# Kernel optimization log

Hardware: AMD Instinct MI355X
Metric: run time of the kernel (lower is better)

Reference implementation:

```python
import jax, jax.numpy as jnp
import numpy as np

N = 100000
E = 400000
NFEAT, NHID, NOUT, NHEAD = 128, 64, 128, 4
HIDDEN = NHID * NHEAD  # 256
SLOPE = 0.2


def gat_conv(x, src, dst, W, a_src, a_dst, b, concat):
    """PyG-style GATConv (eval mode, self-loops already appended to src/dst).
    x: [N, Fin]; W: [Fin, H*C]; a_src/a_dst: [H, C]; b: [H*C] or [C]."""
    H, C = a_src.shape
    h = (x @ W).reshape(N, H, C)                      # [N,H,C]
    al_s = (h * a_src).sum(-1)                        # [N,H] per-node src score
    al_d = (h * a_dst).sum(-1)                        # [N,H] per-node dst score
    e = jax.nn.leaky_relu(al_s[src] + al_d[dst], SLOPE)  # [Et,H]
    # segment softmax over incoming edges of each dst node
    m = jax.ops.segment_max(e, dst, num_segments=N)
    m = jnp.where(jnp.isfinite(m), m, 0.0)
    ex = jnp.exp(e - m[dst])
    denom = jax.ops.segment_sum(ex, dst, num_segments=N)
    alpha = ex / (denom[dst] + 1e-16)                 # [Et,H]
    msg = alpha[:, :, None] * h[src]                  # [Et,H,C]
    out = jax.ops.segment_sum(msg, dst, num_segments=N)  # [N,H,C]
    out = out.reshape(N, H * C) if concat else out.mean(axis=1)
    return out + b


def setup_inputs() -> dict:
    key = jax.random.key(0)
    ks = jax.random.split(key, 16)
    x = jax.random.normal(ks[0], (N, NFEAT), dtype=jnp.float32)
    edge_index = jax.random.randint(ks[1], (2, E), 0, N, dtype=jnp.int64)
    s = 0.1
    inp = {
        'x': x, 'edge_index': edge_index,
        # layer 0: nfeat -> nhid x nhead (concat)
        'W0': jax.random.normal(ks[2], (NFEAT, HIDDEN), jnp.float32) * s,
        'as0': jax.random.normal(ks[3], (NHEAD, NHID), jnp.float32) * s,
        'ad0': jax.random.normal(ks[4], (NHEAD, NHID), jnp.float32) * s,
        'b0': jnp.zeros((HIDDEN,), jnp.float32),
        # layer 1: hidden -> nhid x nhead (concat)
        'W1': jax.random.normal(ks[5], (HIDDEN, HIDDEN), jnp.float32) * s,
        'as1': jax.random.normal(ks[6], (NHEAD, NHID), jnp.float32) * s,
        'ad1': jax.random.normal(ks[7], (NHEAD, NHID), jnp.float32) * s,
        'b1': jnp.zeros((HIDDEN,), jnp.float32),
        # output layer: hidden -> nout, heads=1, concat=False
        'W2': jax.random.normal(ks[8], (HIDDEN, NOUT), jnp.float32) * s,
        'as2': jax.random.normal(ks[9], (1, NOUT), jnp.float32) * s,
        'ad2': jax.random.normal(ks[10], (1, NOUT), jnp.float32) * s,
        'b2': jnp.zeros((NOUT,), jnp.float32),
    }
    return inp


def reference(x, edge_index, W0, as0, ad0, b0, W1, as1, ad1, b1, W2, as2, ad2, b2):
    # PyG GATConv adds self-loops by default; edge set is shared across layers.
    loop = jnp.arange(N, dtype=edge_index.dtype)
    src = jnp.concatenate([edge_index[0], loop])
    dst = jnp.concatenate([edge_index[1], loop])
    # dropout inactive in eval mode
    h = jax.nn.elu(gat_conv(x, src, dst, W0, as0, ad0, b0, concat=True))
    h = jax.nn.elu(gat_conv(h, src, dst, W1, as1, ad1, b1, concat=True))
    out = gat_conv(h, src, dst, W2, as2, ad2, b2, concat=False)
    return out
```

## Files before the change

### kernel.cpp

```cpp
#include <hip/hip_runtime.h>
#include <cmath>

#define NN 100000
#define EE 400000
#define ET (EE + NN)
#define SLOPE 0.2f

typedef __attribute__((ext_vector_type(8))) short short8;
typedef __attribute__((ext_vector_type(4))) float floatx4;

__device__ __forceinline__ float b2f(ushort u) {
    union { unsigned int i; float f; } v; v.i = ((unsigned int)u) << 16; return v.f;
}
__device__ __forceinline__ ushort f2b(float f) {
    union { float f; unsigned int i; } v; v.f = f;
    unsigned int r = v.i + 0x7FFFu + ((v.i >> 16) & 1u);
    return (ushort)(r >> 16);
}

__global__ __launch_bounds__(256) void count_deg(const int* __restrict__ ei, int* __restrict__ deg) {
    int e = blockIdx.x * 256 + threadIdx.x;
    if (e < EE) atomicAdd(&deg[ei[EE + e]], 1);
}

__global__ __launch_bounds__(256) void scan1(const int* __restrict__ deg, int* __restrict__ incl,
                                             int* __restrict__ bsums) {
    __shared__ int ts[256];
    int b = blockIdx.x, t = threadIdx.x;
    int base = b * 1024 + t * 4;
    int v[4];
#pragma unroll
    for (int i = 0; i < 4; i++) {
        int n = base + i;
        v[i] = (n < NN) ? (deg[n] + 1) : 0;
    }
    int s = 0;
#pragma unroll
    for (int i = 0; i < 4; i++) { s += v[i]; v[i] = s; }
    ts[t] = s;
    __syncthreads();
    for (int off = 1; off < 256; off <<= 1) {
        int x = (t >= off) ? ts[t - off] : 0;
        __syncthreads();
        ts[t] += x;
        __syncthreads();
    }
    int excl = ts[t] - s;
#pragma unroll
    for (int i = 0; i < 4; i++) {
        int n = base + i;
        if (n < NN) incl[n] = v[i] + excl;
    }
    if (t == 255) bsums[b] = ts[255];
}

__global__ __launch_bounds__(128) void scan2(int* __restrict__ bsums, int nblk) {
    __shared__ int ts[128];
    int t = threadIdx.x;
    int v = (t < nblk) ? bsums[t] : 0;
    ts[t] = v;
    __syncthreads();
    for (int off = 1; off < 128; off <<= 1) {
        int x = (t >= off) ? ts[t - off] : 0;
        __syncthreads();
        ts[t] += x;
        __syncthreads();
    }
    if (t < nblk) bsums[t] = ts[t] - v;
}

__global__ __launch_bounds__(256) void scan3(const int* __restrict__ incl, const int* __restrict__ deg,
                                             const int* __restrict__ bsums, int* __restrict__ row_ptr,
                                             int* __restrict__ cursor) {
    int n = blockIdx.x * 256 + threadIdx.x;
    if (n < NN) {
        int rp = incl[n] - (deg[n] + 1) + bsums[n >> 10];
        row_ptr[n] = rp;
        cursor[n] = rp;
    }
    if (n == 0) row_ptr[NN] = ET;
}

__global__ __launch_bounds__(256) void scatter(const int* __restrict__ ei, int* __restrict__ cursor,
                                               int* __restrict__ col) {
    int e = blockIdx.x * 256 + threadIdx.x;
    if (e < EE) {
        int d = ei[EE + e];
        int p = atomicAdd(&cursor[d], 1);
        col[p] = ei[e];
    }
}

__global__ __launch_bounds__(256) void selfloop(const int* __restrict__ cursor, int* __restrict__ col) {
    int n = blockIdx.x * 256 + threadIdx.x;
    if (n < NN) col[cursor[n]] = n;
}

__global__ __launch_bounds__(256) void cast_to_bf16(const float* __restrict__ in,
                                                    ushort* __restrict__ out, int n4) {
    int i = blockIdx.x * 256 + threadIdx.x;
    if (i < n4) {
        float4 v = ((const float4*)in)[i];
        ushort4 o;
        o.x = f2b(v.x); o.y = f2b(v.y); o.z = f2b(v.z); o.w = f2b(v.w);
        ((ushort4*)out)[i] = o;
    }
}

__global__ __launch_bounds__(256) void transpose_cast(const float* __restrict__ W,
                                                      ushort* __restrict__ Wt, int K, int N) {
    int idx = blockIdx.x * 256 + threadIdx.x;
    if (idx < N * K) {
        int n = idx / K, k = idx % K;
        Wt[idx] = f2b(W[(size_t)k * N + n]);
    }
}

#define LP 40
__global__ __launch_bounds__(256) void gemm_bf16(const ushort* __restrict__ A,
                                                 const ushort* __restrict__ Bt,
                                                 ushort* __restrict__ C,
                                                 int M, int K, int N) {
    __shared__ ushort As[128 * LP];
    __shared__ ushort Bs[128 * LP];
    int tid = threadIdx.x;
    int bm = blockIdx.x * 128;
    int bn = blockIdx.y * 128;
    int wave = tid >> 6, lane = tid & 63;
    int wm = (wave >> 1) * 64, wn = (wave & 1) * 64;

    floatx4 acc[4][4];
#pragma unroll
    for (int i = 0; i < 4; i++)
#pragma unroll
        for (int j = 0; j < 4; j++) acc[i][j] = (floatx4)0.f;

    int r = tid >> 1;
    int c = (tid & 1) * 16;

    int frow = lane & 15;
    int kq = (lane >> 4) * 8;

    for (int k0 = 0; k0 < K; k0 += 32) {
        uint4 a0, a1;
        if (bm + r < M) {
            const uint4* ap = (const uint4*)(A + (size_t)(bm + r) * K + k0 + c);
            a0 = ap[0]; a1 = ap[1];
        } else {
            a0 = make_uint4(0, 0, 0, 0); a1 = a0;
        }
        *(uint4*)&As[r * LP + c]     = a0;
        *(uint4*)&As[r * LP + c + 8] = a1;

        const uint4* bp = (const uint4*)(Bt + (size_t)(bn + r) * K + k0 + c);
        *(uint4*)&Bs[r * LP + c]     = bp[0];
        *(uint4*)&Bs[r * LP + c + 8] = bp[1];

        __syncthreads();

        short8 afr[4], bfr[4];
#pragma unroll
        for (int i = 0; i < 4; i++)
            afr[i] = *(const short8*)&As[(wm + i * 16 + frow) * LP + kq];
#pragma unroll
        for (int j = 0; j < 4; j++)
            bfr[j] = *(const short8*)&Bs[(wn + j * 16 + frow) * LP + kq];
#pragma unroll
        for (int i = 0; i < 4; i++)
#pragma unroll
            for (int j = 0; j < 4; j++)
                acc[i][j] = __builtin_amdgcn_mfma_f32_16x16x32_bf16(afr[i], bfr[j], acc[i][j], 0, 0, 0);

        __syncthreads();
    }

    int ccol = bn + wn + (lane & 15);
    int crow = bm + wm + (lane >> 4) * 4;
#pragma unroll
    for (int i = 0; i < 4; i++) {
#pragma unroll
        for (int reg = 0; reg < 4; reg++) {
            int row = crow + i * 16 + reg;
            if (row < M) {
#pragma unroll
                for (int j = 0; j < 4; j++)
                    C[(size_t)row * N + ccol + j * 16] = f2b(acc[i][j][reg]);
            }
        }
    }
}

template <int H, int HC>
__global__ __launch_bounds__(256) void scores_k(const ushort* __restrict__ h,
                                                const float* __restrict__ a_s,
                                                const float* __restrict__ a_d,
                                                float* __restrict__ als,
                                                float* __restrict__ ald) {
    constexpr int CP = HC / 64;
    constexpr int GS = 64 / H;
    int wv = threadIdx.x >> 6, lane = threadIdx.x & 63;
    int n = blockIdx.x * 4 + wv;
    if (n >= NN) return;
    const uint* p = (const uint*)(h + (size_t)n * HC + lane * CP);
    float s = 0.f, d = 0.f;
#pragma unroll
    for (int q = 0; q < CP / 2; q++) {
        uint u = p[q];
        int ch = lane * CP + 2 * q;
        float v0 = b2f((ushort)(u & 0xffff)), v1 = b2f((ushort)(u >> 16));
        s += v0 * a_s[ch] + v1 * a_s[ch + 1];
        d += v0 * a_d[ch] + v1 * a_d[ch + 1];
    }
#pragma unroll
    for (int off = 1; off < GS; off <<= 1) {
        s += __shfl_xor(s, off, 64);
        d += __shfl_xor(d, off, 64);
    }
    if ((lane & (GS - 1)) == 0) {
        int head = lane / GS;
        als[n * H + head] = s;
        ald[n * H + head] = d;
    }
}

template <int H, int HC, bool ELU_ACT, bool OUT_BF16>
__global__ __launch_bounds__(256) void aggregate(const ushort* __restrict__ hlin,
                                                 const float* __restrict__ als,
                                                 const float* __restrict__ ald,
                                                 const int* __restrict__ row_ptr,
                                                 const int* __restrict__ col,
                                                 const float* __restrict__ bias,
                                                 void* __restrict__ outv) {
    constexpr int CP = HC / 64;
    constexpr int GS = 64 / H;
    int wv = threadIdx.x >> 6, lane = threadIdx.x & 63;
    int dst = blockIdx.x * 4 + wv;
    if (dst >= NN) return;
    int rs = row_ptr[dst], re = row_ptr[dst + 1];
    int deg = re - rs;
    int eg = lane & (GS - 1);
    int head = lane / GS;
    float ad = ald[dst * H + head];

    float acc[CP];
#pragma unroll
    for (int j = 0; j < CP; j++) acc[j] = 0.f;

    uint laneoff = (uint)(lane * CP);

    if (deg <= GS) {
        int src = 0;
        float s = -1e30f;
        if (eg < deg) {
            src = col[rs + eg];
            float sc = als[src * H + head] + ad;
            s = sc > 0.f ? sc : SLOPE * sc;
        }
        float m = s;
#pragma unroll
        for (int off = 1; off < GS; off <<= 1) m = fmaxf(m, __shfl_xor(m, off, 64));
        float e = (eg < deg) ? __expf(s - m) : 0.f;
        float sum = e;
#pragma unroll
        for (int off = 1; off < GS; off <<= 1) sum += __shfl_xor(sum, off, 64);
        float w = e * (1.0f / (sum + 1e-16f));

        int hbase = head * GS;
        int d = 0;
        for (; d + 4 <= deg; d += 4) {
            int s0 = __shfl(src, d, 64),     s1 = __shfl(src, d + 1, 64);
            int s2 = __shfl(src, d + 2, 64), s3 = __shfl(src, d + 3, 64);
            float w0 = __shfl(w, hbase + d, 64),     w1 = __shfl(w, hbase + d + 1, 64);
            float w2 = __shfl(w, hbase + d + 2, 64), w3 = __shfl(w, hbase + d + 3, 64);
            const uint* p0 = (const uint*)(hlin + (uint)s0 * HC + laneoff);
            const uint* p1 = (const uint*)(hlin + (uint)s1 * HC + laneoff);
            const uint* p2 = (const uint*)(hlin + (uint)s2 * HC + laneoff);
            const uint* p3 = (const uint*)(hlin + (uint)s3 * HC + laneoff);
            uint u0[CP / 2], u1[CP / 2], u2[CP / 2], u3[CP / 2];
#pragma unroll
            for (int q = 0; q < CP / 2; q++) { u0[q] = p0[q]; u1[q] = p1[q]; u2[q] = p2[q]; u3[q] = p3[q]; }
#pragma unroll
            for (int q = 0; q < CP / 2; q++) {
                acc[2*q]   += w0 * b2f((ushort)(u0[q] & 0xffff)) + w1 * b2f((ushort)(u1[q] & 0xffff))
                            + w2 * b2f((ushort)(u2[q] & 0xffff)) + w3 * b2f((ushort)(u3[q] & 0xffff));
                acc[2*q+1] += w0 * b2f((ushort)(u0[q] >> 16)) + w1 * b2f((ushort)(u1[q] >> 16))
                            + w2 * b2f((ushort)(u2[q] >> 16)) + w3 * b2f((ushort)(u3[q] >> 16));
            }
        }
        for (; d < deg; d++) {
            int sd = __shfl(src, d, 64);
            float wd = __shfl(w, hbase + d, 64);
            const uint* p = (const uint*)(hlin + (uint)sd * HC + laneoff);
#pragma unroll
            for (int q = 0; q < CP / 2; q++) {
                uint u = p[q];
                acc[2*q]   += wd * b2f((ushort)(u & 0xffff));
                acc[2*q+1] += wd * b2f((ushort)(u >> 16));
            }
        }
    } else {
        float m = -1e30f;
        for (int e2 = eg; e2 < deg; e2 += GS) {
            int sc0 = col[rs + e2];
            float sc = als[sc0 * H + head] + ad;
            sc = sc > 0.f ? sc : SLOPE * sc;
            m = fmaxf(m, sc);
        }
#pragma unroll
        for (int off = 1; off < GS; off <<= 1) m = fmaxf(m, __shfl_xor(m, off, 64));
        float sum = 0.f;
        for (int e2 = eg; e2 < deg; e2 += GS) {
            int sc0 = col[rs + e2];
            float sc = als[sc0 * H + head] + ad;
            sc = sc > 0.f ? sc : SLOPE * sc;
            sum += __expf(sc - m);
        }
#pragma unroll
        for (int off = 1; off < GS; off <<= 1) sum += __shfl_xor(sum, off, 64);
        float inv = 1.0f / (sum + 1e-16f);
        for (int d = 0; d < deg; d++) {
            int sd = col[rs + d];
            float sc = als[sd * H + head] + ad;
            sc = sc > 0.f ? sc : SLOPE * sc;
            float wd = __expf(sc - m) * inv;
            const uint* p = (const uint*)(hlin + (uint)sd * HC + laneoff);
#pragma unroll
            for (int q = 0; q < CP / 2; q++) {
                uint u = p[q];
                acc[2*q]   += wd * b2f((ushort)(u & 0xffff));
                acc[2*q+1] += wd * b2f((ushort)(u >> 16));
            }
        }
    }

#pragma unroll
    for (int j = 0; j < CP; j++) {
        float v = acc[j] + bias[lane * CP + j];
        if (ELU_ACT) v = v > 0.f ? v : (__expf(v) - 1.0f);
        acc[j] = v;
    }
    if (OUT_BF16) {
        ushort* outp = (ushort*)outv + (size_t)dst * HC + laneoff;
        uint pk[CP / 2];
#pragma unroll
        for (int q = 0; q < CP / 2; q++)
            pk[q] = (uint)f2b(acc[2*q]) | ((uint)f2b(acc[2*q+1]) << 16);
#pragma unroll
        for (int q = 0; q < CP / 2; q++) ((uint*)outp)[q] = pk[q];
    } else {
        float* outp = (float*)outv + (size_t)dst * HC + laneoff;
#pragma unroll
        for (int j = 0; j < CP; j++) outp[j] = acc[j];
    }
}

extern "C" void kernel_launch(void* const* d_in, const int* in_sizes, int n_in,
                              void* d_out, int out_size, void* d_ws, size_t ws_size,
                              hipStream_t stream) {
    const float* x   = (const float*)d_in[0];
    const int*   ei  = (const int*)d_in[1];
    const float* W0  = (const float*)d_in[2];
    const float* as0 = (const float*)d_in[3];
    const float* ad0 = (const float*)d_in[4];
    const float* b0  = (const float*)d_in[5];
    const float* W1  = (const float*)d_in[6];
    const float* as1 = (const float*)d_in[7];
    const float* ad1 = (const float*)d_in[8];
    const float* b1  = (const float*)d_in[9];
    const float* W2  = (const float*)d_in[10];
    const float* as2 = (const float*)d_in[11];
    const float* ad2 = (const float*)d_in[12];
    const float* b2  = (const float*)d_in[13];
    float* out = (float*)d_out;

    char* ws = (char*)d_ws;
    size_t off = 0;
    auto alloc = [&](size_t bytes) {
        void* p = ws + off;
        off += (bytes + 255) & ~(size_t)255;
        return p;
    };
    ushort* xb   = (ushort*)alloc((size_t)NN * 128 * 2);
    ushort* h    = (ushort*)alloc((size_t)NN * 256 * 2);
    ushort* actB = (ushort*)alloc((size_t)NN * 256 * 2);
    ushort* actC = (ushort*)alloc((size_t)NN * 256 * 2);
    ushort* Wt0  = (ushort*)alloc((size_t)256 * 128 * 2);
    ushort* Wt1  = (ushort*)alloc((size_t)256 * 256 * 2);
    ushort* Wt2  = (ushort*)alloc((size_t)128 * 256 * 2);
    float* als   = (float*)alloc((size_t)NN * 4 * 4);
    float* ald   = (float*)alloc((size_t)NN * 4 * 4);
    int* deg     = (int*)alloc((size_t)NN * 4);
    int* incl    = (int*)alloc((size_t)NN * 4);
    int* row_ptr = (int*)alloc((size_t)(NN + 1) * 4);
    int* cursor  = (int*)alloc((size_t)NN * 4);
    int* col     = (int*)alloc((size_t)ET * 4);
    int* bsums   = (int*)alloc(128 * 4);

    const int NBLK = (NN + 1023) / 1024;

    hipMemsetAsync(deg, 0, (size_t)NN * 4, stream);
    count_deg<<<(EE + 255) / 256, 256, 0, stream>>>(ei, deg);
    scan1<<<NBLK, 256, 0, stream>>>(deg, incl, bsums);
    scan2<<<1, 128, 0, stream>>>(bsums, NBLK);
    scan3<<<(NN + 255) / 256, 256, 0, stream>>>(incl, deg, bsums, row_ptr, cursor);
    scatter<<<(EE + 255) / 256, 256, 0, stream>>>(ei, cursor, col);
    selfloop<<<(NN + 255) / 256, 256, 0, stream>>>(cursor, col);

    cast_to_bf16<<<(NN * 128 / 4 + 255) / 256, 256, 0, stream>>>(x, xb, NN * 128 / 4);
    transpose_cast<<<(256 * 128 + 255) / 256, 256, 0, stream>>>(W0, Wt0, 128, 256);
    transpose_cast<<<(256 * 256 + 255) / 256, 256, 0, stream>>>(W1, Wt1, 256, 256);
    transpose_cast<<<(128 * 256 + 255) / 256, 256, 0, stream>>>(W2, Wt2, 256, 128);

    const int GM = (NN + 127) / 128;
    const int NB4 = (NN + 3) / 4;

    gemm_bf16<<<dim3(GM, 2), 256, 0, stream>>>(xb, Wt0, h, NN, 128, 256);
    scores_k<4, 256><<<NB4, 256, 0, stream>>>(h, as0, ad0, als, ald);
    aggregate<4, 256, true, true><<<NB4, 256, 0, stream>>>(h, als, ald, row_ptr, col, b0, actB);

    gemm_bf16<<<dim3(GM, 2), 256, 0, stream>>>(actB, Wt1, h, NN, 256, 256);
    scores_k<4, 256><<<NB4, 256, 0, stream>>>(h, as1, ad1, als, ald);
    aggregate<4, 256, true, true><<<NB4, 256, 0, stream>>>(h, als, ald, row_ptr, col, b1, actC);

    gemm_bf16<<<dim3(GM, 1), 256, 0, stream>>>(actC, Wt2, h, NN, 256, 128);
    scores_k<1, 128><<<NB4, 256, 0, stream>>>(h, as2, ad2, als, ald);
    aggregate<1, 128, false, false><<<NB4, 256, 0, stream>>>(h, als, ald, row_ptr, col, b2, out);
}
```

Baseline: 470.9 us.

## Fuse attention score computation into GEMM epilogue and use direct global-to-LDS loads

```diff
diff --git a/kernel.cpp b/kernel.cpp
--- a/kernel.cpp
+++ b/kernel.cpp
@@ -2,6 +2,7 @@
 #include <cmath>
 
 #define NN 100000
+#define NP 100096
 #define EE 400000
 #define ET (EE + NN)
 #define SLOPE 0.2f
@@ -17,6 +18,10 @@
     unsigned int r = v.i + 0x7FFFu + ((v.i >> 16) & 1u);
     return (ushort)(r >> 16);
 }
+
+#define GLL16(g, l) __builtin_amdgcn_global_load_lds( \
+    (const __attribute__((address_space(1))) unsigned int*)(g), \
+    (__attribute__((address_space(3))) unsigned int*)(l), 16, 0, 0)
 
 __global__ __launch_bounds__(256) void count_deg(const int* __restrict__ ei, int* __restrict__ deg) {
     int e = blockIdx.x * 256 + threadIdx.x;
@@ -116,18 +121,21 @@
     }
 }
 
-#define LP 40
 __global__ __launch_bounds__(256) void gemm_bf16(const ushort* __restrict__ A,
                                                  const ushort* __restrict__ Bt,
                                                  ushort* __restrict__ C,
-                                                 int M, int K, int N) {
-    __shared__ ushort As[128 * LP];
-    __shared__ ushort Bs[128 * LP];
+                                                 const float* __restrict__ a_s,
+                                                 const float* __restrict__ a_d,
+                                                 float* __restrict__ als,
+                                                 float* __restrict__ ald,
+                                                 int M, int K, int N, int H) {
+    __shared__ ushort As[8 * 512];
+    __shared__ ushort Bs[8 * 512];
     int tid = threadIdx.x;
-    int bm = blockIdx.x * 128;
-    int bn = blockIdx.y * 128;
     int wave = tid >> 6, lane = tid & 63;
+    int bm = blockIdx.x * 128, bn = blockIdx.y * 128;
     int wm = (wave >> 1) * 64, wn = (wave & 1) * 64;
+    int frow = lane & 15, kq = (lane >> 4) * 8;
 
     floatx4 acc[4][4];
 #pragma unroll
@@ -135,36 +143,33 @@
 #pragma unroll
         for (int j = 0; j < 4; j++) acc[i][j] = (floatx4)0.f;
 
-    int r = tid >> 1;
-    int c = (tid & 1) * 16;
-
-    int frow = lane & 15;
-    int kq = (lane >> 4) * 8;
+    int s0 = wave * 2;
+    const ushort* gA0 = A + (size_t)(bm + s0 * 16 + frow) * K + kq;
+    const ushort* gA1 = gA0 + (size_t)16 * K;
+    const ushort* gB0 = Bt + (size_t)(bn + s0 * 16 + frow) * K + kq;
+    const ushort* gB1 = gB0 + (size_t)16 * K;
+    ushort* lA0 = As + s0 * 512;
+    ushort* lA1 = As + (s0 + 1) * 512;
+    ushort* lB0 = Bs + s0 * 512;
+    ushort* lB1 = Bs + (s0 + 1) * 512;
+
+    int sa = wm >> 4;
+    int sb = wn >> 4;
 
     for (int k0 = 0; k0 < K; k0 += 32) {
-        uint4 a0, a1;
-        if (bm + r < M) {
-            const uint4* ap = (const uint4*)(A + (size_t)(bm + r) * K + k0 + c);
-            a0 = ap[0]; a1 = ap[1];
-        } else {
-            a0 = make_uint4(0, 0, 0, 0); a1 = a0;
-        }
-        *(uint4*)&As[r * LP + c]     = a0;
-        *(uint4*)&As[r * LP + c + 8] = a1;
-
-        const uint4* bp = (const uint4*)(Bt + (size_t)(bn + r) * K + k0 + c);
-        *(uint4*)&Bs[r * LP + c]     = bp[0];
-        *(uint4*)&Bs[r * LP + c + 8] = bp[1];
-
+        GLL16(gA0 + k0, lA0);
+        GLL16(gA1 + k0, lA1);
+        GLL16(gB0 + k0, lB0);
+        GLL16(gB1 + k0, lB1);
         __syncthreads();
 
         short8 afr[4], bfr[4];
 #pragma unroll
         for (int i = 0; i < 4; i++)
-            afr[i] = *(const short8*)&As[(wm + i * 16 + frow) * LP + kq];
+            afr[i] = *(const short8*)&As[(sa + i) * 512 + lane * 8];
 #pragma unroll
         for (int j = 0; j < 4; j++)
-            bfr[j] = *(const short8*)&Bs[(wn + j * 16 + frow) * LP + kq];
+            bfr[j] = *(const short8*)&Bs[(sb + j) * 512 + lane * 8];
 #pragma unroll
         for (int i = 0; i < 4; i++)
 #pragma unroll
@@ -174,7 +179,7 @@
         __syncthreads();
     }
 
-    int ccol = bn + wn + (lane & 15);
+    int ccol = bn + wn + frow;
     int crow = bm + wm + (lane >> 4) * 4;
 #pragma unroll
     for (int i = 0; i < 4; i++) {
@@ -188,38 +193,37 @@
             }
         }
     }
-}
-
-template <int H, int HC>
-__global__ __launch_bounds__(256) void scores_k(const ushort* __restrict__ h,
-                                                const float* __restrict__ a_s,
-                                                const float* __restrict__ a_d,
-                                                float* __restrict__ als,
-                                                float* __restrict__ ald) {
-    constexpr int CP = HC / 64;
-    constexpr int GS = 64 / H;
-    int wv = threadIdx.x >> 6, lane = threadIdx.x & 63;
-    int n = blockIdx.x * 4 + wv;
-    if (n >= NN) return;
-    const uint* p = (const uint*)(h + (size_t)n * HC + lane * CP);
-    float s = 0.f, d = 0.f;
-#pragma unroll
-    for (int q = 0; q < CP / 2; q++) {
-        uint u = p[q];
-        int ch = lane * CP + 2 * q;
-        float v0 = b2f((ushort)(u & 0xffff)), v1 = b2f((ushort)(u >> 16));
-        s += v0 * a_s[ch] + v1 * a_s[ch + 1];
-        d += v0 * a_d[ch] + v1 * a_d[ch + 1];
-    }
-#pragma unroll
-    for (int off = 1; off < GS; off <<= 1) {
-        s += __shfl_xor(s, off, 64);
-        d += __shfl_xor(d, off, 64);
-    }
-    if ((lane & (GS - 1)) == 0) {
-        int head = lane / GS;
-        als[n * H + head] = s;
-        ald[n * H + head] = d;
+
+    int Cc = N / H;
+    int hd = (bn + wn) / Cc;
+    float avs[4], avd[4];
+#pragma unroll
+    for (int j = 0; j < 4; j++) {
+        avs[j] = a_s[bn + wn + frow + j * 16];
+        avd[j] = a_d[bn + wn + frow + j * 16];
+    }
+#pragma unroll
+    for (int i = 0; i < 4; i++) {
+#pragma unroll
+        for (int reg = 0; reg < 4; reg++) {
+            float ps = 0.f, pd = 0.f;
+#pragma unroll
+            for (int j = 0; j < 4; j++) {
+                float v = acc[i][j][reg];
+                ps += v * avs[j];
+                pd += v * avd[j];
+            }
+#pragma unroll
+            for (int off = 1; off < 16; off <<= 1) {
+                ps += __shfl_xor(ps, off, 64);
+                pd += __shfl_xor(pd, off, 64);
+            }
+            int row = crow + i * 16 + reg;
+            if ((lane & 15) == 0 && row < M) {
+                atomicAdd(&als[row * H + hd], ps);
+                atomicAdd(&ald[row * H + hd], pd);
+            }
+        }
     }
 }
 
@@ -380,10 +384,10 @@
         off += (bytes + 255) & ~(size_t)255;
         return p;
     };
-    ushort* xb   = (ushort*)alloc((size_t)NN * 128 * 2);
-    ushort* h    = (ushort*)alloc((size_t)NN * 256 * 2);
-    ushort* actB = (ushort*)alloc((size_t)NN * 256 * 2);
-    ushort* actC = (ushort*)alloc((size_t)NN * 256 * 2);
+    ushort* xb   = (ushort*)alloc((size_t)NP * 128 * 2);
+    ushort* h    = (ushort*)alloc((size_t)NP * 256 * 2);
+    ushort* actB = (ushort*)alloc((size_t)NP * 256 * 2);
+    ushort* actC = (ushort*)alloc((size_t)NP * 256 * 2);
     ushort* Wt0  = (ushort*)alloc((size_t)256 * 128 * 2);
     ushort* Wt1  = (ushort*)alloc((size_t)256 * 256 * 2);
     ushort* Wt2  = (ushort*)alloc((size_t)128 * 256 * 2);
@@ -411,18 +415,22 @@
     transpose_cast<<<(256 * 256 + 255) / 256, 256, 0, stream>>>(W1, Wt1, 256, 256);
     transpose_cast<<<(128 * 256 + 255) / 256, 256, 0, stream>>>(W2, Wt2, 256, 128);
 
-    const int GM = (NN + 127) / 128;
+    const int GM = NP / 128;
     const int NB4 = (NN + 3) / 4;
-
-    gemm_bf16<<<dim3(GM, 2), 256, 0, stream>>>(xb, Wt0, h, NN, 128, 256);
-    scores_k<4, 256><<<NB4, 256, 0, stream>>>(h, as0, ad0, als, ald);
+    const size_t ALB = (size_t)NN * 4 * 4;
+
+    hipMemsetAsync(als, 0, ALB, stream);
+    hipMemsetAsync(ald, 0, ALB, stream);
+    gemm_bf16<<<dim3(GM, 2), 256, 0, stream>>>(xb, Wt0, h, as0, ad0, als, ald, NN, 128, 256, 4);
     aggregate<4, 256, true, true><<<NB4, 256, 0, stream>>>(h, als, ald, row_ptr, col, b0, actB);
 
-    gemm_bf16<<<dim3(GM, 2), 256, 0, stream>>>(actB, Wt1, h, NN, 256, 256);
-    scores_k<4, 256><<<NB4, 256, 0, stream>>>(h, as1, ad1, als, ald);
+    hipMemsetAsync(als, 0, ALB, stream);
+    hipMemsetAsync(ald, 0, ALB, stream);
+    gemm_bf16<<<dim3(GM, 2), 256, 0, stream>>>(actB, Wt1, h, as1, ad1, als, ald, NN, 256, 256, 4);
     aggregate<4, 256, true, true><<<NB4, 256, 0, stream>>>(h, als, ald, row_ptr, col, b1, actC);
 
-    gemm_bf16<<<dim3(GM, 1), 256, 0, stream>>>(actC, Wt2, h, NN, 256, 128);
-    scores_k<1, 128><<<NB4, 256, 0, stream>>>(h, as2, ad2, als, ald);
+    hipMemsetAsync(als, 0, ALB, stream);
+    hipMemsetAsync(ald, 0, ALB, stream);
+    gemm_bf16<<<dim3(GM, 1), 256, 0, stream>>>(actC, Wt2, h, as2, ad2, als, ald, NN, 256, 128, 1);
     aggregate<1, 128, false, false><<<NB4, 256, 0, stream>>>(h, als, ald, row_ptr, col, b2, out);
 }
```

New measurement: 530.2 us. 1.13x slower.
